# Kernel tuning notes

Measured on AMD Instinct MI355X. Metric: run time of the kernel, lower is better.

## Reference

```python
import jax, jax.numpy as jnp
import numpy as np

B, N, C, H = 8, 2048, 512, 8
D = C // H  # head_dim = 64

def rope(t):
    # t: (B, H, T, D); rotate even/odd interleaved pairs
    T = t.shape[2]
    inv_freq = 1.0 / (10000.0 ** (jnp.arange(0, D, 2, dtype=t.dtype) / D))  # (D/2,)
    pos = jnp.arange(T, dtype=t.dtype)
    freqs = pos[:, None] * inv_freq[None, :]            # (T, D/2)
    cos, sin = jnp.cos(freqs), jnp.sin(freqs)           # broadcast over (B,H)
    t_un = t[..., 0::2]
    t_ev = t[..., 1::2]
    r_un = t_un * cos - t_ev * sin
    r_ev = t_un * sin + t_ev * cos
    # interleave back: (..., D/2, 2) -> (..., D)
    return jnp.stack([r_un, r_ev], axis=-1).reshape(t.shape)

def setup_inputs() -> dict:
    key = jax.random.key(0)
    k1, k2, k3, k4 = jax.random.split(key, 4)
    x = jax.random.normal(k1, (B, N, C), dtype=jnp.float32)
    mask = jax.random.normal(k2, (B, N), dtype=jnp.float32)
    W_qkv = jax.random.normal(k3, (3 * C, C), dtype=jnp.float32) * (1.0 / np.sqrt(C))
    W_proj = jax.random.normal(k4, (C, C), dtype=jnp.float32) * (1.0 / np.sqrt(C))
    b_proj = jnp.zeros((C,), dtype=jnp.float32)
    return {"x": x, "mask": mask, "W_qkv": W_qkv, "W_proj": W_proj,
            "b_proj": b_proj, "num_cls_token": 1}

def reference(x, mask, W_qkv, W_proj, b_proj, num_cls_token):
    scale = D ** (-0.5)
    qkv = jnp.einsum('bnc,fc->bnf', x, W_qkv)             # (B,N,3C)
    qkv = qkv.reshape(B, N, 3, H, D).transpose(2, 0, 3, 1, 4)  # (3,B,H,N,D)
    q, k, v = qkv[0], qkv[1], qkv[2]
    nc = num_cls_token
    if nc > 0:
        q = jnp.concatenate([q[:, :, :nc], rope(q[:, :, nc:])], axis=2)
        k = jnp.concatenate([k[:, :, :nc], rope(k[:, :, nc:])], axis=2)
    else:
        q, k = rope(q), rope(k)
    attn = jnp.einsum('bhnd,bhmd->bhnm', q * scale, k)    # (B,H,N,N)
    attn = attn + mask[:, None, None, :] + mask[:, None, :, None]
    attn = jax.nn.softmax(attn, axis=-1)
    out = jnp.einsum('bhnm,bhmd->bhnd', attn, v)          # (B,H,N,D)
    out = out.transpose(0, 2, 1, 3).reshape(B, N, C)
    return out @ W_proj.T + b_proj
```

## Files before the change

kernel.cpp:

```cpp
#include <hip/hip_runtime.h>
#include <cmath>

#define BB 8
#define NN 2048
#define CC 512
#define HH 8
#define DD 64
#define FF 1536
#define MM (BB*NN)

typedef _Float16 half_t;
typedef __attribute__((ext_vector_type(8))) _Float16 half8;
typedef __attribute__((ext_vector_type(4))) _Float16 half4;
typedef __attribute__((ext_vector_type(4))) float floatx4;
typedef __attribute__((ext_vector_type(16))) float floatx16;
typedef __attribute__((ext_vector_type(4))) float fx4;

#define LOG2E 1.44269504088896f

typedef const __attribute__((address_space(1))) unsigned int* gas_ptr;
typedef __attribute__((address_space(3))) unsigned int* las_ptr;
__device__ __forceinline__ void gld16(const half_t* g, half_t* l) {
  __builtin_amdgcn_global_load_lds((gas_ptr)g, (las_ptr)l, 16, 0, 0);
}

__global__ __launch_bounds__(256) void cvt_kernel(
    const float* __restrict__ s, half_t* __restrict__ d, int n8) {
  int i = blockIdx.x * 256 + threadIdx.x;
  if (i < n8) {
    float4 a = ((const float4*)s)[i * 2], b = ((const float4*)s)[i * 2 + 1];
    half8 h;
    h[0] = (half_t)a.x; h[1] = (half_t)a.y; h[2] = (half_t)a.z; h[3] = (half_t)a.w;
    h[4] = (half_t)b.x; h[5] = (half_t)b.y; h[6] = (half_t)b.z; h[7] = (half_t)b.w;
    ((half8*)d)[i] = h;
  }
}

__global__ __launch_bounds__(256) void qkv_mfma_kernel(
    const half_t* __restrict__ Ah,
    const half_t* __restrict__ Bh,
    const int*   __restrict__ ncp,
    half_t* __restrict__ Qh, half_t* __restrict__ Kh, half_t* __restrict__ Vt)
{
  __shared__ union {
    struct { half_t A[128 * 32]; half_t B[128 * 32]; } s;
    half_t T[4][64 * 68];
  } sm;

  const int tid  = threadIdx.x;
  const int wave = tid >> 6, lane = tid & 63;
  const int L15  = lane & 15, quad = lane >> 4;
  const int wm = (wave & 1) * 64, wn = (wave >> 1) * 64;
  const int m0 = blockIdx.x * 128;
  const int f0 = blockIdx.y * 128;

  const int srow = lane >> 2;
  const int scolh = (lane & 3) * 8;
  const half_t* Ag = Ah + (size_t)(m0 + wave * 16 + srow) * CC + scolh;
  const half_t* Bg = Bh + (size_t)(f0 + wave * 16 + srow) * CC + scolh;
  half_t* Al = &sm.s.A[(wave * 16) * 32];
  half_t* Bl = &sm.s.B[(wave * 16) * 32];

  floatx4 acc[4][4];
#pragma unroll
  for (int i = 0; i < 4; ++i)
#pragma unroll
    for (int j = 0; j < 4; ++j) acc[i][j] = (floatx4){0.f, 0.f, 0.f, 0.f};

  for (int k0 = 0; k0 < CC; k0 += 32) {
    __syncthreads();
    gld16(Ag + k0,            Al);
    gld16(Ag + k0 + 64 * CC,  Al + 64 * 32);
    gld16(Bg + k0,            Bl);
    gld16(Bg + k0 + 64 * CC,  Bl + 64 * 32);
    __syncthreads();
    half8 af[4], bf[4];
#pragma unroll
    for (int mi = 0; mi < 4; ++mi)
      af[mi] = *(const half8*)&sm.s.A[(wm + mi * 16 + L15) * 32 + quad * 8];
#pragma unroll
    for (int ni = 0; ni < 4; ++ni)
      bf[ni] = *(const half8*)&sm.s.B[(wn + ni * 16 + L15) * 32 + quad * 8];
#pragma unroll
    for (int mi = 0; mi < 4; ++mi)
#pragma unroll
      for (int ni = 0; ni < 4; ++ni)
        acc[mi][ni] = __builtin_amdgcn_mfma_f32_16x16x32_f16(af[mi], bf[ni], acc[mi][ni], 0, 0, 0);
  }

  const int which = f0 >> 9;
  const int b     = m0 >> 11;
  const int n_base = (m0 & 2047) + wm;

  if (which < 2) {
    const int nc = *ncp;
    half_t* dst = which ? Kh : Qh;
    const float qscale = which ? 1.0f : (0.125f * LOG2E);
#pragma unroll
    for (int ni = 0; ni < 4; ++ni) {
      const int f = f0 + wn + ni * 16 + L15;
      const int h = (f >> 6) & 7;
      const int d = f & 63;
      const float invf = __powf(10000.0f, -(float)(d & ~1) * (1.0f / 64.0f));
      const float sgn = (d & 1) ? 1.0f : -1.0f;
#pragma unroll
      for (int mi = 0; mi < 4; ++mi)
#pragma unroll
        for (int r = 0; r < 4; ++r) {
          const int n = n_base + mi * 16 + quad * 4 + r;
          float v = acc[mi][ni][r];
          float p = __shfl_xor(v, 1, 64);
          if (n >= nc) {
            float sv, cv;
            __sincosf((float)(n - nc) * invf, &sv, &cv);
            v = v * cv + sgn * p * sv;
          }
          dst[(((size_t)(b * HH + h) * NN + n) << 6) + d] = (half_t)(v * qscale);
        }
    }
  } else {
    __syncthreads();
#pragma unroll
    for (int ni = 0; ni < 4; ++ni)
#pragma unroll
      for (int mi = 0; mi < 4; ++mi)
#pragma unroll
        for (int r = 0; r < 4; ++r)
          sm.T[wave][(ni * 16 + L15) * 68 + mi * 16 + quad * 4 + r] = (half_t)acc[mi][ni][r];
    __syncthreads();
    const int h = ((f0 + wn) >> 6) & 7;
    const size_t gbase = ((size_t)(b * HH + h) * DD + lane) * NN + n_base;
#pragma unroll
    for (int c = 0; c < 8; ++c)
      *(half8*)(Vt + gbase + c * 8) = *(const half8*)&sm.T[wave][lane * 68 + c * 8];
  }
}

#define EXP2_OFF 4.3280851f
__global__ __launch_bounds__(256, 4) void flash_mfma_kernel(
    const half_t* __restrict__ Qh,
    const half_t* __restrict__ Kh,
    const half_t* __restrict__ Vt,
    const float*  __restrict__ mask,
    half_t* __restrict__ O)
{
  __shared__ half_t KV[2][2][64 * 64];

  const int tid  = threadIdx.x;
  const int wave = tid >> 6;
  const int lane = tid & 63;
  const int l31  = lane & 31;
  const int hi   = lane >> 5;
  const int l7   = lane & 7;

  const int bid  = blockIdx.x;
  const int xcd  = bid & 7;
  const int slot = bid >> 3;
  const int qt   = slot & 15;
  const int head = (slot >> 4) * 8 + xcd;
  const int b    = head >> 3;
  const int h    = head & 7;

  const half_t* Kt_base = Kh + ((((size_t)b * HH + h) * NN) << 6);
  const half_t* Vt_base = Vt + (((size_t)b * HH + h) * DD) * NN;

  half8 qf[4];
  {
    const half_t* Qp =
        Qh + ((((size_t)b * HH + h) * NN + qt * 128 + wave * 32 + l31) << 6) + hi * 8;
#pragma unroll
    for (int kd = 0; kd < 4; ++kd) qf[kd] = *(const half8*)(Qp + kd * 16);
  }

  const int r8  = lane >> 3;
  const int dof = ((l7 ^ r8) << 3);
  const half_t* kg0 = Kt_base + (((size_t)(wave * 16 + r8)) << 6) + dof;
  const half_t* kg1 = kg0 + (8 << 6);
  const half_t* vg0 = Vt_base + (size_t)(wave * 16 + r8) * NN + dof;
  const half_t* vg1 = vg0 + (size_t)8 * NN;

  int adK[4], adV[4];
#pragma unroll
  for (int c = 0; c < 4; ++c) {
    const int sw = ((((c << 1) | hi) ^ l7) << 4);
    adK[c] = l31 * 128 + sw;
    adV[c] = 8192 + l31 * 128 + sw;
  }
  const char* L = (const char*)KV;

  floatx16 acc[2];
#pragma unroll
  for (int dt = 0; dt < 2; ++dt)
#pragma unroll
    for (int r = 0; r < 16; ++r) acc[dt][r] = 0.f;
  float l_part = 0.f;

  const float* mkb = mask + (size_t)b * NN + hi * 4;

  gld16(kg0, &KV[0][0][wave * 1024]);
  gld16(kg1, &KV[0][0][wave * 1024 + 512]);
  gld16(vg0, &KV[0][1][wave * 1024]);
  gld16(vg1, &KV[0][1][wave * 1024 + 512]);
  __syncthreads();

#pragma unroll 1
  for (int kt = 0; kt < NN / 64; ++kt) {
    if (kt != NN / 64 - 1) {
      kg0 += 4096; kg1 += 4096; vg0 += 64; vg1 += 64;
      const int nb = (kt & 1) ^ 1;
      gld16(kg0, &KV[nb][0][wave * 1024]);
      gld16(kg1, &KV[nb][0][wave * 1024 + 512]);
      gld16(vg0, &KV[nb][1][wave * 1024]);
      gld16(vg1, &KV[nb][1][wave * 1024 + 512]);
    }

#pragma unroll
    for (int t = 0; t < 2; ++t) {
      fx4 m4[4];
#pragma unroll
      for (int r2 = 0; r2 < 4; ++r2)
        m4[r2] = *(const fx4*)(mkb + t * 32 + r2 * 8);

      floatx16 S;
#pragma unroll
      for (int r = 0; r < 16; ++r) S[r] = 0.f;
#pragma unroll
      for (int kd = 0; kd < 4; ++kd) {
        half8 kf = *(const half8*)(L + (adK[kd] + t * 4096));
        S = __builtin_amdgcn_mfma_f32_32x32x16_f16(kf, qf[kd], S, 0, 0, 0);
      }

#pragma unroll
      for (int r = 0; r < 16; ++r) {
        float p = __builtin_amdgcn_exp2f(fmaf(m4[r >> 2][r & 3], LOG2E, S[r] - EXP2_OFF));
        l_part += p;
        S[r] = p;
      }

      unsigned W[4][2];
#pragma unroll
      for (int r2 = 0; r2 < 4; ++r2)
#pragma unroll
        for (int u = 0; u < 2; ++u) {
          union { half_t hh[2]; unsigned w; } pk;
          pk.hh[0] = (half_t)S[r2 * 4 + 2 * u];
          pk.hh[1] = (half_t)S[r2 * 4 + 2 * u + 1];
          W[r2][u] = pk.w;
        }

#pragma unroll
      for (int ksl = 0; ksl < 2; ++ksl) {
        unsigned A0 = W[2 * ksl][0],     A1 = W[2 * ksl][1];
        unsigned B0 = W[2 * ksl + 1][0], B1 = W[2 * ksl + 1][1];
        unsigned pA0 = __shfl_xor(A0, 32, 64), pA1 = __shfl_xor(A1, 32, 64);
        unsigned pB0 = __shfl_xor(B0, 32, 64), pB1 = __shfl_xor(B1, 32, 64);
        union { unsigned u[4]; half8 v; } pw;
        pw.u[0] = hi ? pB0 : A0;
        pw.u[1] = hi ? pB1 : A1;
        pw.u[2] = hi ? B0 : pA0;
        pw.u[3] = hi ? B1 : pA1;
        const int ks = t * 2 + ksl;
#pragma unroll
        for (int dt = 0; dt < 2; ++dt) {
          half8 vf = *(const half8*)(L + (adV[ks] + dt * 4096));
          acc[dt] = __builtin_amdgcn_mfma_f32_32x32x16_f16(pw.v, vf, acc[dt], 0, 0, 0);
        }
      }
    }

    mkb += 64;
    __syncthreads();
#pragma unroll
    for (int c = 0; c < 4; ++c) { adK[c] ^= 16384; adV[c] ^= 16384; }
  }

  l_part += __shfl_xor(l_part, 32, 64);

  const size_t orow = (size_t)b * NN + qt * 128 + wave * 32;
#pragma unroll
  for (int r = 0; r < 16; ++r) {
    const int ql  = (r & 3) + 8 * (r >> 2) + 4 * hi;
    const float iv = 1.0f / __shfl(l_part, ql, 64);
    const size_t ro = ((orow + ql) << 9) + (h << 6) + l31;
    O[ro]      = (half_t)(acc[0][r] * iv);
    O[ro + 32] = (half_t)(acc[1][r] * iv);
  }
}

__global__ __launch_bounds__(256) void proj_mfma_kernel(
    const half_t* __restrict__ Ah,
    const half_t* __restrict__ Bh,
    const float* __restrict__ bias,
    float* __restrict__ out)
{
  __shared__ half_t As[128 * 32];
  __shared__ half_t Bs[128 * 32];

  const int tid  = threadIdx.x;
  const int wave = tid >> 6, lane = tid & 63;
  const int L15  = lane & 15, quad = lane >> 4;
  const int wm = (wave & 1) * 64, wn = (wave >> 1) * 64;
  const int m0 = blockIdx.x * 128;
  const int f0 = blockIdx.y * 128;

  const int srow = lane >> 2;
  const int scolh = (lane & 3) * 8;
  const half_t* Ag = Ah + (size_t)(m0 + wave * 16 + srow) * CC + scolh;
  const half_t* Bg = Bh + (size_t)(f0 + wave * 16 + srow) * CC + scolh;
  half_t* Al = &As[(wave * 16) * 32];
  half_t* Bl = &Bs[(wave * 16) * 32];

  floatx4 acc[4][4];
#pragma unroll
  for (int i = 0; i < 4; ++i)
#pragma unroll
    for (int j = 0; j < 4; ++j) acc[i][j] = (floatx4){0.f, 0.f, 0.f, 0.f};

  for (int k0 = 0; k0 < CC; k0 += 32) {
    __syncthreads();
    gld16(Ag + k0,           Al);
    gld16(Ag + k0 + 64 * CC, Al + 64 * 32);
    gld16(Bg + k0,           Bl);
    gld16(Bg + k0 + 64 * CC, Bl + 64 * 32);
    __syncthreads();
    half8 af[4], bf[4];
#pragma unroll
    for (int mi = 0; mi < 4; ++mi)
      af[mi] = *(const half8*)&As[(wm + mi * 16 + L15) * 32 + quad * 8];
#pragma unroll
    for (int ni = 0; ni < 4; ++ni)
      bf[ni] = *(const half8*)&Bs[(wn + ni * 16 + L15) * 32 + quad * 8];
#pragma unroll
    for (int mi = 0; mi < 4; ++mi)
#pragma unroll
      for (int ni = 0; ni < 4; ++ni)
        acc[mi][ni] = __builtin_amdgcn_mfma_f32_16x16x32_f16(af[mi], bf[ni], acc[mi][ni], 0, 0, 0);
  }

#pragma unroll
  for (int ni = 0; ni < 4; ++ni) {
    const int f = f0 + wn + ni * 16 + L15;
    const float bv = bias[f];
#pragma unroll
    for (int mi = 0; mi < 4; ++mi)
#pragma unroll
      for (int r = 0; r < 4; ++r)
        out[(size_t)(m0 + wm + mi * 16 + quad * 4 + r) * CC + f] = acc[mi][ni][r] + bv;
  }
}

extern "C" void kernel_launch(void* const* d_in, const int* in_sizes, int n_in,
                              void* d_out, int out_size, void* d_ws, size_t ws_size,
                              hipStream_t stream) {
  const float* x     = (const float*)d_in[0];
  const float* mask  = (const float*)d_in[1];
  const float* Wqkv  = (const float*)d_in[2];
  const float* Wproj = (const float*)d_in[3];
  const float* bproj = (const float*)d_in[4];
  const int*   ncp   = (const int*)d_in[5];
  float* out = (float*)d_out;

  const size_t per = (size_t)BB * HH * NN * DD;
  half_t* xh  = (half_t*)d_ws;
  half_t* Wqh = xh + (size_t)MM * CC;
  half_t* Wph = Wqh + (size_t)FF * CC;
  half_t* Qh  = Wph + (size_t)CC * CC;
  half_t* Kh  = Qh + per;
  half_t* Vt  = Kh + per;
  half_t* Oh  = Vt + per;

  cvt_kernel<<<dim3(MM * CC / 8 / 256), 256, 0, stream>>>(x, xh, MM * CC / 8);
  cvt_kernel<<<dim3(FF * CC / 8 / 256), 256, 0, stream>>>(Wqkv, Wqh, FF * CC / 8);
  cvt_kernel<<<dim3(CC * CC / 8 / 256), 256, 0, stream>>>(Wproj, Wph, CC * CC / 8);

  qkv_mfma_kernel<<<dim3(MM / 128, FF / 128), 256, 0, stream>>>(xh, Wqh, ncp, Qh, Kh, Vt);
  flash_mfma_kernel<<<dim3(BB * HH * (NN / 128)), 256, 0, stream>>>(Qh, Kh, Vt, mask, Oh);
  proj_mfma_kernel<<<dim3(MM / 128, CC / 128), 256, 0, stream>>>(Oh, Wph, bproj, out);
}
```

Measured before the change: 280.7 us.

## Restructure attention K/V pipeline with manual two-stage unroll and partial waitcnt

Unrolls the KV loop by two with static LDS buffer indices and issues the next tile's global-to-LDS loads after each compute stage. It replaces full __syncthreads drains with s_waitcnt vmcnt(4), so one tile's loads can stay in flight while the other is computed. It also wraps MFMA sections in s_setprio(1) and places sched_barriers to pin instruction order. The aim is to hide global load latency and reduce barrier stalls, at the cost of fragile hand-written vmcnt/barrier logic.

```diff
diff --git a/kernel.cpp b/kernel.cpp
--- a/kernel.cpp
+++ b/kernel.cpp
@@ -174,17 +174,14 @@
 
   const int r8  = lane >> 3;
   const int dof = ((l7 ^ r8) << 3);
-  const half_t* kg0 = Kt_base + (((size_t)(wave * 16 + r8)) << 6) + dof;
-  const half_t* kg1 = kg0 + (8 << 6);
-  const half_t* vg0 = Vt_base + (size_t)(wave * 16 + r8) * NN + dof;
-  const half_t* vg1 = vg0 + (size_t)8 * NN;
+  const half_t* kbase = Kt_base + (((size_t)(wave * 16 + r8)) << 6) + dof;
+  const half_t* vbase = Vt_base + (size_t)(wave * 16 + r8) * NN + dof;
 
   int adK[4], adV[4];
 #pragma unroll
   for (int c = 0; c < 4; ++c) {
-    const int sw = ((((c << 1) | hi) ^ l7) << 4);
-    adK[c] = l31 * 128 + sw;
-    adV[c] = 8192 + l31 * 128 + sw;
+    adK[c] = l31 * 128 + ((((c << 1) | hi) ^ l7) << 4);
+    adV[c] = 8192 + l31 * 128 + ((((c << 1) | hi) ^ l7) << 4);
   }
   const char* L = (const char*)KV;
 
@@ -197,82 +194,105 @@
 
   const float* mkb = mask + (size_t)b * NN + hi * 4;
 
-  gld16(kg0, &KV[0][0][wave * 1024]);
-  gld16(kg1, &KV[0][0][wave * 1024 + 512]);
-  gld16(vg0, &KV[0][1][wave * 1024]);
-  gld16(vg1, &KV[0][1][wave * 1024 + 512]);
-  __syncthreads();
+#define STAGE(c, koff, voff)                                                  \
+  {                                                                           \
+    gld16(kbase + (koff),          &KV[c][0][wave * 1024]);                   \
+    gld16(kbase + (koff) + 512,    &KV[c][0][wave * 1024 + 512]);             \
+    gld16(vbase + (voff),          &KV[c][1][wave * 1024]);                   \
+    gld16(vbase + (voff) + 8 * NN, &KV[c][1][wave * 1024 + 512]);             \
+  }
+
+#define COMPUTE(c, moff)                                                      \
+  _Pragma("unroll")                                                           \
+  for (int t = 0; t < 2; ++t) {                                               \
+    fx4 m4[4];                                                                \
+    _Pragma("unroll")                                                         \
+    for (int r2 = 0; r2 < 4; ++r2)                                            \
+      m4[r2] = *(const fx4*)(mkb + (moff) + t * 32 + r2 * 8);                 \
+    floatx16 S;                                                               \
+    _Pragma("unroll") for (int r = 0; r < 16; ++r) S[r] = 0.f;                \
+    __builtin_amdgcn_s_setprio(1);                                            \
+    _Pragma("unroll")                                                         \
+    for (int kd = 0; kd < 4; ++kd) {                                          \
+      half8 kf = *(const half8*)(L + (adK[kd] + (c) * 16384 + t * 4096));     \
+      S = __builtin_amdgcn_mfma_f32_32x32x16_f16(kf, qf[kd], S, 0, 0, 0);     \
+    }                                                                         \
+    __builtin_amdgcn_s_setprio(0);                                            \
+    _Pragma("unroll")                                                         \
+    for (int r = 0; r < 16; ++r) {                                            \
+      float p = __builtin_amdgcn_exp2f(fmaf(m4[r >> 2][r & 3], LOG2E, S[r] - EXP2_OFF)); \
+      l_part += p;                                                            \
+      S[r] = p;                                                               \
+    }                                                                         \
+    unsigned W[4][2];                                                         \
+    _Pragma("unroll")                                                         \
+    for (int r2 = 0; r2 < 4; ++r2)                                            \
+      _Pragma("unroll")                                                       \
+      for (int u = 0; u < 2; ++u) {                                           \
+        union { half_t hh[2]; unsigned w; } pk;                               \
+        pk.hh[0] = (half_t)S[r2 * 4 + 2 * u];                                 \
+        pk.hh[1] = (half_t)S[r2 * 4 + 2 * u + 1];                             \
+        W[r2][u] = pk.w;                                                      \
+      }                                                                       \
+    _Pragma("unroll")                                                         \
+    for (int ksl = 0; ksl < 2; ++ksl) {                                       \
+      unsigned A0 = W[2 * ksl][0],     A1 = W[2 * ksl][1];                    \
+      unsigned B0 = W[2 * ksl + 1][0], B1 = W[2 * ksl + 1][1];                \
+      unsigned pA0 = __shfl_xor(A0, 32, 64), pA1 = __shfl_xor(A1, 32, 64);    \
+      unsigned pB0 = __shfl_xor(B0, 32, 64), pB1 = __shfl_xor(B1, 32, 64);    \
+      union { unsigned u4[4]; half8 v; } pw;                                  \
+      pw.u4[0] = hi ? pB0 : A0;                                               \
+      pw.u4[1] = hi ? pB1 : A1;                                               \
+      pw.u4[2] = hi ? B0 : pA0;                                               \
+      pw.u4[3] = hi ? B1 : pA1;                                               \
+      const int ks = t * 2 + ksl;                                             \
+      __builtin_amdgcn_s_setprio(1);                                          \
+      _Pragma("unroll")                                                       \
+      for (int dt = 0; dt < 2; ++dt) {                                        \
+        half8 vf = *(const half8*)(L + (adV[ks] + (c) * 16384 + dt * 4096));  \
+        acc[dt] = __builtin_amdgcn_mfma_f32_32x32x16_f16(pw.v, vf, acc[dt], 0, 0, 0); \
+      }                                                                       \
+      __builtin_amdgcn_s_setprio(0);                                          \
+    }                                                                         \
+  }
+
+  STAGE(0, 0, 0)
+  STAGE(1, 4096, 64)
+  asm volatile("s_waitcnt vmcnt(4)");
+  __builtin_amdgcn_s_barrier();
+  __builtin_amdgcn_sched_barrier(0);
+  kbase += 8192; vbase += 128;
 
 #pragma unroll 1
-  for (int kt = 0; kt < NN / 64; ++kt) {
-    if (kt != NN / 64 - 1) {
-      kg0 += 4096; kg1 += 4096; vg0 += 64; vg1 += 64;
-      const int nb = (kt & 1) ^ 1;
-      gld16(kg0, &KV[nb][0][wave * 1024]);
-      gld16(kg1, &KV[nb][0][wave * 1024 + 512]);
-      gld16(vg0, &KV[nb][1][wave * 1024]);
-      gld16(vg1, &KV[nb][1][wave * 1024 + 512]);
-    }
-
-#pragma unroll
-    for (int t = 0; t < 2; ++t) {
-      fx4 m4[4];
-#pragma unroll
-      for (int r2 = 0; r2 < 4; ++r2)
-        m4[r2] = *(const fx4*)(mkb + t * 32 + r2 * 8);
-
-      floatx16 S;
-#pragma unroll
-      for (int r = 0; r < 16; ++r) S[r] = 0.f;
-#pragma unroll
-      for (int kd = 0; kd < 4; ++kd) {
-        half8 kf = *(const half8*)(L + (adK[kd] + t * 4096));
-        S = __builtin_amdgcn_mfma_f32_32x32x16_f16(kf, qf[kd], S, 0, 0, 0);
-      }
-
-#pragma unroll
-      for (int r = 0; r < 16; ++r) {
-        float p = __builtin_amdgcn_exp2f(fmaf(m4[r >> 2][r & 3], LOG2E, S[r] - EXP2_OFF));
-        l_part += p;
-        S[r] = p;
-      }
-
-      unsigned W[4][2];
-#pragma unroll
-      for (int r2 = 0; r2 < 4; ++r2)
-#pragma unroll
-        for (int u = 0; u < 2; ++u) {
-          union { half_t hh[2]; unsigned w; } pk;
-          pk.hh[0] = (half_t)S[r2 * 4 + 2 * u];
-          pk.hh[1] = (half_t)S[r2 * 4 + 2 * u + 1];
-          W[r2][u] = pk.w;
-        }
-
-#pragma unroll
-      for (int ksl = 0; ksl < 2; ++ksl) {
-        unsigned A0 = W[2 * ksl][0],     A1 = W[2 * ksl][1];
-        unsigned B0 = W[2 * ksl + 1][0], B1 = W[2 * ksl + 1][1];
-        unsigned pA0 = __shfl_xor(A0, 32, 64), pA1 = __shfl_xor(A1, 32, 64);
-        unsigned pB0 = __shfl_xor(B0, 32, 64), pB1 = __shfl_xor(B1, 32, 64);
-        union { unsigned u[4]; half8 v; } pw;
-        pw.u[0] = hi ? pB0 : A0;
-        pw.u[1] = hi ? pB1 : A1;
-        pw.u[2] = hi ? B0 : pA0;
-        pw.u[3] = hi ? B1 : pA1;
-        const int ks = t * 2 + ksl;
-#pragma unroll
-        for (int dt = 0; dt < 2; ++dt) {
-          half8 vf = *(const half8*)(L + (adV[ks] + dt * 4096));
-          acc[dt] = __builtin_amdgcn_mfma_f32_32x32x16_f16(pw.v, vf, acc[dt], 0, 0, 0);
-        }
-      }
-    }
-
-    mkb += 64;
-    __syncthreads();
-#pragma unroll
-    for (int c = 0; c < 4; ++c) { adK[c] ^= 16384; adV[c] ^= 16384; }
-  }
+  for (int kt2 = 0; kt2 < 15; ++kt2) {
+    COMPUTE(0, 0)
+    __builtin_amdgcn_sched_barrier(0);
+    __builtin_amdgcn_s_barrier();
+    STAGE(0, 0, 0)
+    asm volatile("s_waitcnt vmcnt(4)");
+    __builtin_amdgcn_s_barrier();
+    __builtin_amdgcn_sched_barrier(0);
+
+    COMPUTE(1, 64)
+    __builtin_amdgcn_sched_barrier(0);
+    __builtin_amdgcn_s_barrier();
+    STAGE(1, 4096, 64)
+    asm volatile("s_waitcnt vmcnt(4)");
+    __builtin_amdgcn_s_barrier();
+    __builtin_amdgcn_sched_barrier(0);
+
+    kbase += 8192; vbase += 128;
+    mkb += 128;
+  }
+
+  COMPUTE(0, 0)
+  asm volatile("s_waitcnt vmcnt(0)");
+  __builtin_amdgcn_s_barrier();
+  __builtin_amdgcn_sched_barrier(0);
+  COMPUTE(1, 64)
+
+#undef STAGE
+#undef COMPUTE
 
   l_part += __shfl_xor(l_part, 32, 64);
 
```

Result: faster. 270.8 us (-3.5%).
